# Optimization experiments

Hardware: AMD Instinct MI355X
Metric: run time of the kernel (lower is better)

## Reference

```python
import jax, jax.numpy as jnp
import numpy as np

B, N, D, H = 16, 512, 256, 8
E_PER = 16384  # edges per graph (avg degree 32)
BN_EPS = 1e-5


def _bn(x, g, b, m, v):
    # BatchNorm1d in eval mode: normalize with running stats
    return (x - m) * (g * jax.lax.rsqrt(v + BN_EPS)) + b


def setup_inputs() -> dict:
    key = jax.random.key(0)
    ks = jax.random.split(key, 32)
    E = B * E_PER
    w = lambda k, s: (jax.random.normal(k, s, jnp.float32) * 0.02)
    # block-diagonal edge list: indices within each graph + graph offset
    src = jax.random.randint(ks[1], (B, E_PER), 0, N)
    dst = jax.random.randint(ks[2], (B, E_PER), 0, N)
    off = (jnp.arange(B) * N)[:, None]
    inp = {
        "x": jax.random.normal(ks[0], (B * N, D), jnp.float32),
        "edge_rows": (src + off).reshape(-1).astype(jnp.int32),
        "edge_cols": (dst + off).reshape(-1).astype(jnp.int32),
        "edge_vals": jax.random.uniform(ks[3], (E,), jnp.float32) * 0.1,
        "w_gcn": w(ks[4], (D, D)),
        "in_proj_w": w(ks[5], (3 * D, D)),
        "in_proj_b": w(ks[6], (3 * D,)),
        "out_proj_w": w(ks[7], (D, D)),
        "out_proj_b": w(ks[8], (D,)),
        "w1": w(ks[9], (4 * D, D)),
        "b1": w(ks[10], (4 * D,)),
        "w2": w(ks[11], (D, 4 * D)),
        "b2": w(ks[12], (D,)),
        "batch_size": B,
        "num_nodes": N,
    }
    for i, name in enumerate(["bn1", "bn2", "bn3"]):
        k4 = jax.random.split(ks[13 + i], 4)
        inp[name + "_g"] = 1.0 + jax.random.uniform(k4[0], (D,), jnp.float32) * 0.1
        inp[name + "_b"] = w(k4[1], (D,))
        inp[name + "_m"] = w(k4[2], (D,))
        inp[name + "_v"] = 1.0 + jax.random.uniform(k4[3], (D,), jnp.float32) * 0.1
    return inp


def reference(x, edge_rows, edge_cols, edge_vals, w_gcn,
              in_proj_w, in_proj_b, out_proj_w, out_proj_b,
              bn1_g, bn1_b, bn1_m, bn1_v,
              bn2_g, bn2_b, bn2_m, bn2_v,
              bn3_g, bn3_b, bn3_m, bn3_v,
              w1, b1, w2, b2, batch_size, num_nodes):
    n_total = x.shape[0]
    dh = D // H
    # --- local GCN: linear -> sparse SpMM (gather/scatter) -> exact GELU ---
    hl = x @ w_gcn.T                                            # (BN, D)
    agg = jax.ops.segment_sum(edge_vals[:, None] * hl[edge_cols],
                              edge_rows, num_segments=n_total)   # (BN, D)
    h_local = jax.nn.gelu(agg, approximate=False)
    x = x + h_local
    x = _bn(x, bn1_g, bn1_b, bn1_m, bn1_v)
    # --- global multi-head self-attention per graph ---
    h = x.reshape(batch_size, num_nodes, D)
    qkv = jnp.einsum('bnd,ed->bne', h, in_proj_w) + in_proj_b    # (B, N, 3D)
    q, k, v = jnp.split(qkv, 3, axis=-1)
    q = q.reshape(batch_size, num_nodes, H, dh)
    k = k.reshape(batch_size, num_nodes, H, dh)
    v = v.reshape(batch_size, num_nodes, H, dh)
    scores = jnp.einsum('bqhd,bkhd->bhqk', q, k) / jnp.sqrt(jnp.float32(dh))
    attn = jax.nn.softmax(scores, axis=-1)
    ctx = jnp.einsum('bhqk,bkhd->bqhd', attn, v).reshape(batch_size, num_nodes, D)
    h_attn = (ctx @ out_proj_w.T + out_proj_b).reshape(n_total, D)
    x = x + h_attn
    x = _bn(x, bn2_g, bn2_b, bn2_m, bn2_v)
    # --- FFN ---
    h_ffn = jax.nn.gelu(x @ w1.T + b1, approximate=False) @ w2.T + b2
    x = x + h_ffn
    x = _bn(x, bn3_g, bn3_b, bn3_m, bn3_v)
    return x
```

## Files before the change

### kernel.cpp

```cpp
#include <hip/hip_runtime.h>
#include <hip/hip_bf16.h>
#include <math.h>

#define D_    256
#define NT_   8192
#define NN_   512
#define B_    16
#define H_    8
#define EPG_  16384
#define BN_EPS 1e-5f

typedef __attribute__((ext_vector_type(8))) short bx8;
typedef __attribute__((ext_vector_type(4))) float fx4;

__device__ __forceinline__ float gelu_exact(float x) {
    return 0.5f * x * (1.0f + erff(x * 0.70710678118654752f));
}

typedef __attribute__((address_space(1))) const unsigned int GU;
typedef __attribute__((address_space(3))) unsigned int LU;
__device__ __forceinline__ void gl_lds16(const void* g, void* l) {
    __builtin_amdgcn_global_load_lds((GU*)g, (LU*)l, 16, 0, 0);
}

template<int TM, int TN, int EPI, int OBF, int RBF>
__global__ __launch_bounds__(256)
void mgemm(const short* __restrict__ A, const short* __restrict__ Bw,
           const float* __restrict__ bias, void* __restrict__ Cout,
           int M, int N, int K,
           long sA, long sB, long sC, long sR,
           const void* __restrict__ resid,
           const float* __restrict__ bng, const float* __restrict__ bnb,
           const float* __restrict__ bnm, const float* __restrict__ bnv)
{
    constexpr int MR = TM / 32, NR = TN / 32;
    constexpr int IA = TM / 16, IB = TN / 16;
    __shared__ short As[TM][32];
    __shared__ short Bs[TN][32];
    const int bz = blockIdx.z;
    A  += (size_t)bz * sA;
    Bw += (size_t)bz * sB;
    const int bm = blockIdx.y * TM, bn = blockIdx.x * TN;
    const int tid = threadIdx.x;
    const int w = tid >> 6, lane = tid & 63;
    const int wm = w >> 1, wn = w & 1;
    const int fr = lane & 15, fk = (lane >> 4) << 3;
    const int srow = lane >> 2, scol = (lane & 3) << 3;
    fx4 acc[MR][NR] = {};

    for (int k0 = 0; k0 < K; k0 += 32) {
        __syncthreads();
        #pragma unroll
        for (int i = w; i < IA + IB; i += 4) {
            if (i < IA)
                gl_lds16(A + (size_t)(bm + i * 16 + srow) * K + k0 + scol,
                         (char*)As + i * 1024);
            else
                gl_lds16(Bw + (size_t)(bn + (i - IA) * 16 + srow) * K + k0 + scol,
                         (char*)Bs + (i - IA) * 1024);
        }
        __syncthreads();
        bx8 af[MR], bf[NR];
        #pragma unroll
        for (int m = 0; m < MR; ++m) af[m] = *(const bx8*)&As[wm * (TM / 2) + m * 16 + fr][fk];
        #pragma unroll
        for (int n = 0; n < NR; ++n) bf[n] = *(const bx8*)&Bs[wn * (TN / 2) + n * 16 + fr][fk];
        #pragma unroll
        for (int m = 0; m < MR; ++m)
            #pragma unroll
            for (int n = 0; n < NR; ++n)
                acc[m][n] = __builtin_amdgcn_mfma_f32_16x16x32_bf16(af[m], bf[n], acc[m][n], 0, 0, 0);
    }

    float* Cf = (float*)Cout + (size_t)bz * sC;
    __hip_bfloat16* Cb = (__hip_bfloat16*)Cout + (size_t)bz * sC;
    const float* Rf = (const float*)resid + (EPI >= 2 ? (size_t)bz * sR : 0);
    const __hip_bfloat16* Rb = (const __hip_bfloat16*)resid + (EPI >= 2 ? (size_t)bz * sR : 0);
    #pragma unroll
    for (int m = 0; m < MR; ++m) {
        #pragma unroll
        for (int n = 0; n < NR; ++n) {
            #pragma unroll
            for (int r = 0; r < 4; ++r) {
                const int gm = bm + wm * (TM / 2) + m * 16 + (lane >> 4) * 4 + r;
                const int gn = bn + wn * (TN / 2) + n * 16 + fr;
                float v = acc[m][n][r];
                if (bias) v += bias[gn];
                if (EPI == 1) v = gelu_exact(v);
                if (EPI == 2 || EPI == 3) {
                    const float rv = RBF ? __bfloat162float(Rb[(size_t)gm * N + gn])
                                         : Rf[(size_t)gm * N + gn];
                    if (EPI == 2) v += rv;
                    else          v = rv + gelu_exact(v);
                    v = (v - bnm[gn]) * (bng[gn] * rsqrtf(bnv[gn] + BN_EPS)) + bnb[gn];
                }
                if (OBF) Cb[(size_t)gm * N + gn] = __float2bfloat16(v);
                else     Cf[(size_t)gm * N + gn] = v;
            }
        }
    }
}

__device__ __forceinline__ void cv4(const float4 v, __hip_bfloat16* d) {
    __hip_bfloat162* dp = (__hip_bfloat162*)d;
    dp[0] = __hip_bfloat162(__float2bfloat16(v.x), __float2bfloat16(v.y));
    dp[1] = __hip_bfloat162(__float2bfloat16(v.z), __float2bfloat16(v.w));
}

__global__ __launch_bounds__(256)
void conv6(const float* __restrict__ x,  const float* __restrict__ wg,
           const float* __restrict__ iw, const float* __restrict__ ow,
           const float* __restrict__ w1, const float* __restrict__ w2,
           __hip_bfloat16* xb, __hip_bfloat16* wgb, __hip_bfloat16* iwb,
           __hip_bfloat16* owb, __hip_bfloat16* w1b, __hip_bfloat16* w2b)
{
    int i = blockIdx.x * 256 + threadIdx.x;
    const float* s; __hip_bfloat16* d; int o;
    if      (i < 524288) { s = x;  d = xb;  o = i; }
    else if (i < 540672) { s = wg; d = wgb; o = i - 524288; }
    else if (i < 589824) { s = iw; d = iwb; o = i - 540672; }
    else if (i < 606208) { s = ow; d = owb; o = i - 589824; }
    else if (i < 671744) { s = w1; d = w1b; o = i - 606208; }
    else                 { s = w2; d = w2b; o = i - 671744; }
    cv4(((const float4*)s)[o], d + (size_t)o * 4);
}

__global__ __launch_bounds__(256)
void convA(const float* __restrict__ s, __hip_bfloat16* __restrict__ d, int n4)
{
    int i = blockIdx.x * 256 + threadIdx.x;
    if (i >= n4) return;
    cv4(((const float4*)s)[i], d + (size_t)i * 4);
}

__global__ __launch_bounds__(256)
void build_S(const int* __restrict__ rows, const int* __restrict__ cols,
             const float* __restrict__ vals, float* __restrict__ SA)
{
    const int e = blockIdx.x * 256 + threadIdx.x;
    const int r = rows[e], c = cols[e];
    const int g = r >> 9;
    atomicAdd(&SA[((size_t)g << 18) + (size_t)(r & 511) * 512 + (c - (g << 9))], vals[e]);
}

__global__ __launch_bounds__(256)
void transp(const __hip_bfloat16* __restrict__ hl, __hip_bfloat16* __restrict__ hlB)
{
    __shared__ short T[64][72];
    const int nt = blockIdx.x, it = blockIdx.y, g = blockIdx.z;
    const int r0 = threadIdx.x >> 3, c8 = (threadIdx.x & 7) << 3;
    #pragma unroll
    for (int u = 0; u < 2; ++u) {
        const int r = r0 + u * 32;
        *(bx8*)&T[r][c8] = *(const bx8*)&hl[(size_t)(g * 512 + it * 64 + r) * 256 + nt * 64 + c8];
    }
    __syncthreads();
    #pragma unroll
    for (int u = 0; u < 2; ++u) {
        const int r = r0 + u * 32;
        bx8 o;
        #pragma unroll
        for (int j = 0; j < 8; ++j) o[j] = T[c8 + j][r];
        *(bx8*)&hlB[((size_t)(g * 256 + nt * 64 + r)) * 512 + it * 64 + c8] = o;
    }
}

__global__ __launch_bounds__(256, 1)
void attn_mfma(const short* __restrict__ qkv, __hip_bfloat16* __restrict__ ctx)
{
    const int qt = blockIdx.x & 7;
    const int h  = (blockIdx.x >> 3) & 7;
    const int b  = blockIdx.x >> 6;
    __shared__ short Ks[512][40];
    __shared__ short Vt[32][520];
    __shared__ short Ps[64][520];
    const int tid = threadIdx.x;
    const int lane = tid & 63, wq = tid >> 6;
    const short* base = qkv + (size_t)b * NN_ * 768;

    {
        const int d0 = (tid & 3) << 3;
        const int k0 = tid >> 2;
        #pragma unroll
        for (int rep = 0; rep < 8; ++rep) {
            const int key = k0 + rep * 64;
            *(bx8*)&Ks[key][d0] =
                *(const bx8*)(base + (size_t)key * 768 + 256 + h * 32 + d0);
        }
    }
    {
        const int d0 = (tid >> 6) << 3;
        const int k0 = tid & 63;
        #pragma unroll
        for (int rep = 0; rep < 8; ++rep) {
            const int key = k0 + rep * 64;
            bx8 vv = *(const bx8*)(base + (size_t)key * 768 + 512 + h * 32 + d0);
            #pragma unroll
            for (int j = 0; j < 8; ++j) Vt[d0 + j][key] = vv[j];
        }
    }
    const int fr = lane & 15, fk = (lane >> 4) << 3;
    const int qrow = qt * 64 + wq * 16 + fr;
    bx8 qf = *(const bx8*)(base + (size_t)qrow * 768 + h * 32 + fk);
    __syncthreads();

    fx4 sc[32];
    #pragma unroll
    for (int nt = 0; nt < 32; ++nt) {
        bx8 kf = *(const bx8*)&Ks[nt * 16 + fr][fk];
        fx4 z = {0.f, 0.f, 0.f, 0.f};
        sc[nt] = __builtin_amdgcn_mfma_f32_16x16x32_bf16(qf, kf, z, 0, 0, 0);
    }

    const float scale = 0.17677669529663687f;
    #pragma unroll
    for (int r = 0; r < 4; ++r) {
        float m = -1e30f;
        #pragma unroll
        for (int nt = 0; nt < 32; ++nt) m = fmaxf(m, sc[nt][r]);
        #pragma unroll
        for (int off = 1; off < 16; off <<= 1)
            m = fmaxf(m, __shfl_xor(m, off, 64));
        const float M = m * scale;
        float s = 0.f;
        #pragma unroll
        for (int nt = 0; nt < 32; ++nt) {
            const float p = __expf(sc[nt][r] * scale - M);
            sc[nt][r] = p;
            s += p;
        }
        #pragma unroll
        for (int off = 1; off < 16; off <<= 1) s += __shfl_xor(s, off, 64);
        const float inv = 1.0f / s;
        const int q = wq * 16 + (lane >> 4) * 4 + r;
        #pragma unroll
        for (int nt = 0; nt < 32; ++nt)
            *(__hip_bfloat16*)&Ps[q][nt * 16 + fr] = __float2bfloat16(sc[nt][r] * inv);
    }

    fx4 oacc[2] = {};
    #pragma unroll
    for (int step = 0; step < 16; ++step) {
        bx8 pf = *(const bx8*)&Ps[wq * 16 + fr][step * 32 + fk];
        #pragma unroll
        for (int nt = 0; nt < 2; ++nt) {
            bx8 vf = *(const bx8*)&Vt[nt * 16 + fr][step * 32 + fk];
            oacc[nt] = __builtin_amdgcn_mfma_f32_16x16x32_bf16(pf, vf, oacc[nt], 0, 0, 0);
        }
    }
    #pragma unroll
    for (int nt = 0; nt < 2; ++nt) {
        #pragma unroll
        for (int r = 0; r < 4; ++r) {
            const int q = qt * 64 + wq * 16 + (lane >> 4) * 4 + r;
            const int d = nt * 16 + fr;
            ctx[(size_t)(b * NN_ + q) * D_ + h * 32 + d] = __float2bfloat16(oacc[nt][r]);
        }
    }
}

extern "C" void kernel_launch(void* const* d_in, const int* in_sizes, int n_in,
                              void* d_out, int out_size, void* d_ws, size_t ws_size,
                              hipStream_t stream) {
    const float* x      = (const float*)d_in[0];
    const int*   erows  = (const int*)d_in[1];
    const int*   ecols  = (const int*)d_in[2];
    const float* evals  = (const float*)d_in[3];
    const float* w_gcn  = (const float*)d_in[4];
    const float* in_w   = (const float*)d_in[5];
    const float* in_b   = (const float*)d_in[6];
    const float* outw   = (const float*)d_in[7];
    const float* outb   = (const float*)d_in[8];
    const float* w1     = (const float*)d_in[9];
    const float* b1     = (const float*)d_in[10];
    const float* w2     = (const float*)d_in[11];
    const float* b2     = (const float*)d_in[12];
    const float* bn1g = (const float*)d_in[15], *bn1b = (const float*)d_in[16];
    const float* bn1m = (const float*)d_in[17], *bn1v = (const float*)d_in[18];
    const float* bn2g = (const float*)d_in[19], *bn2b = (const float*)d_in[20];
    const float* bn2m = (const float*)d_in[21], *bn2v = (const float*)d_in[22];
    const float* bn3g = (const float*)d_in[23], *bn3b = (const float*)d_in[24];
    const float* bn3m = (const float*)d_in[25], *bn3v = (const float*)d_in[26];

    short* wsS = (short*)d_ws;
    __hip_bfloat16* xb    = (__hip_bfloat16*)(wsS + 0);
    __hip_bfloat16* wgcnb = (__hip_bfloat16*)(wsS + 2097152);
    __hip_bfloat16* iwb   = (__hip_bfloat16*)(wsS + 2162688);
    __hip_bfloat16* owb   = (__hip_bfloat16*)(wsS + 2359296);
    __hip_bfloat16* w1b   = (__hip_bfloat16*)(wsS + 2424832);
    __hip_bfloat16* w2b   = (__hip_bfloat16*)(wsS + 2686976);
    short* hl   = wsS + 2949120;
    short* hlB  = wsS + 5046272;
    short* x1b  = wsS + 7143424;
    short* ctxb = wsS + 9240576;
    short* x2b  = wsS + 11337728;
    short* h1b  = wsS + 13434880;
    short* SAb  = wsS + 21823488;
    float* SA   = (float*)(wsS + 26017792);
    short* qkvb = wsS + 26017792;
    float* out  = (float*)d_out;

    dim3 blk(256);
    conv6<<<dim3(2880), blk, 0, stream>>>(x, w_gcn, in_w, outw, w1, w2,
                                          xb, wgcnb, iwb, owb, w1b, w2b);
    hipMemsetAsync(SA, 0, (size_t)16 * 512 * 512 * 4, stream);
    build_S<<<dim3(1024), blk, 0, stream>>>(erows, ecols, evals, SA);
    convA<<<dim3(4096), blk, 0, stream>>>(SA, (__hip_bfloat16*)SAb, 1048576);
    mgemm<64,64,0,1,0><<<dim3(4, 128), blk, 0, stream>>>((const short*)xb, (const short*)wgcnb,
        nullptr, hl, NT_, D_, D_, 0,0,0,0, nullptr, nullptr, nullptr, nullptr, nullptr);
    transp<<<dim3(4, 8, 16), blk, 0, stream>>>((const __hip_bfloat16*)hl, (__hip_bfloat16*)hlB);
    mgemm<64,64,3,1,0><<<dim3(4, 8, 16), blk, 0, stream>>>(SAb, hlB, nullptr, x1b,
        512, D_, 512, 262144, 131072, 131072, 131072,
        x, bn1g, bn1b, bn1m, bn1v);
    mgemm<128,64,0,1,0><<<dim3(12, 64), blk, 0, stream>>>(x1b, (const short*)iwb, in_b, qkvb,
        NT_, 3 * D_, D_, 0,0,0,0, nullptr, nullptr, nullptr, nullptr, nullptr);
    attn_mfma<<<dim3(1024), blk, 0, stream>>>(qkvb, (__hip_bfloat16*)ctxb);
    mgemm<64,64,2,1,1><<<dim3(4, 128), blk, 0, stream>>>(ctxb, (const short*)owb, outb, x2b,
        NT_, D_, D_, 0,0,0,0, x1b, bn2g, bn2b, bn2m, bn2v);
    mgemm<128,64,1,1,0><<<dim3(16, 64), blk, 0, stream>>>(x2b, (const short*)w1b, b1, h1b,
        NT_, 4 * D_, D_, 0,0,0,0, nullptr, nullptr, nullptr, nullptr, nullptr);
    mgemm<64,64,2,0,1><<<dim3(4, 128), blk, 0, stream>>>(h1b, (const short*)w2b, b2, out,
        NT_, D_, 4 * D_, 0,0,0,0, x2b, bn3g, bn3b, bn3m, bn3v);
}
```

Before: 258.0 us.

## Deepen GEMM K-step to 64 with XOR-swizzled LDS, enlarge tiles, swizzle attention blocks

The GEMM kernel now stages 64-wide K slices per iteration into LDS, using an XOR swizzle on 16-byte chunks to avoid bank conflicts, and issues two MFMA sub-steps per barrier pair. This halves the number of synchronisation rounds and should reduce LDS conflicts. The QKV and FFN-up GEMMs switch to 128x128 tiles for more register reuse, at the cost of fewer blocks. The attention kernel remaps block indices so that consecutively launched blocks spread across different graphs and heads.

```diff
diff --git a/kernel.cpp b/kernel.cpp
--- a/kernel.cpp
+++ b/kernel.cpp
@@ -34,9 +34,9 @@
            const float* __restrict__ bnm, const float* __restrict__ bnv)
 {
     constexpr int MR = TM / 32, NR = TN / 32;
-    constexpr int IA = TM / 16, IB = TN / 16;
-    __shared__ short As[TM][32];
-    __shared__ short Bs[TN][32];
+    constexpr int NIA = TM / 8, NIB = TN / 8;
+    __shared__ short As[TM][64];
+    __shared__ short Bs[TN][64];
     const int bz = blockIdx.z;
     A  += (size_t)bz * sA;
     Bw += (size_t)bz * sB;
@@ -44,32 +44,43 @@
     const int tid = threadIdx.x;
     const int w = tid >> 6, lane = tid & 63;
     const int wm = w >> 1, wn = w & 1;
-    const int fr = lane & 15, fk = (lane >> 4) << 3;
-    const int srow = lane >> 2, scol = (lane & 3) << 3;
+    const int fr = lane & 15;
+    const int srow = lane >> 3;
+    const int scol = (((lane & 7) ^ (srow & 7)) << 3);
     fx4 acc[MR][NR] = {};
 
-    for (int k0 = 0; k0 < K; k0 += 32) {
+    for (int k0 = 0; k0 < K; k0 += 64) {
         __syncthreads();
         #pragma unroll
-        for (int i = w; i < IA + IB; i += 4) {
-            if (i < IA)
-                gl_lds16(A + (size_t)(bm + i * 16 + srow) * K + k0 + scol,
+        for (int i = w; i < NIA + NIB; i += 4) {
+            if (i < NIA)
+                gl_lds16(A + (size_t)(bm + i * 8 + srow) * K + k0 + scol,
                          (char*)As + i * 1024);
             else
-                gl_lds16(Bw + (size_t)(bn + (i - IA) * 16 + srow) * K + k0 + scol,
-                         (char*)Bs + (i - IA) * 1024);
+                gl_lds16(Bw + (size_t)(bn + (i - NIA) * 8 + srow) * K + k0 + scol,
+                         (char*)Bs + (i - NIA) * 1024);
         }
         __syncthreads();
-        bx8 af[MR], bf[NR];
-        #pragma unroll
-        for (int m = 0; m < MR; ++m) af[m] = *(const bx8*)&As[wm * (TM / 2) + m * 16 + fr][fk];
-        #pragma unroll
-        for (int n = 0; n < NR; ++n) bf[n] = *(const bx8*)&Bs[wn * (TN / 2) + n * 16 + fr][fk];
-        #pragma unroll
-        for (int m = 0; m < MR; ++m)
-            #pragma unroll
-            for (int n = 0; n < NR; ++n)
-                acc[m][n] = __builtin_amdgcn_mfma_f32_16x16x32_bf16(af[m], bf[n], acc[m][n], 0, 0, 0);
+        #pragma unroll
+        for (int ks = 0; ks < 2; ++ks) {
+            const int sl = (ks << 2) | (lane >> 4);
+            bx8 af[MR], bf[NR];
+            #pragma unroll
+            for (int m = 0; m < MR; ++m) {
+                const int row = wm * (TM / 2) + m * 16 + fr;
+                af[m] = *(const bx8*)&As[row][(sl ^ (row & 7)) << 3];
+            }
+            #pragma unroll
+            for (int n = 0; n < NR; ++n) {
+                const int row = wn * (TN / 2) + n * 16 + fr;
+                bf[n] = *(const bx8*)&Bs[row][(sl ^ (row & 7)) << 3];
+            }
+            #pragma unroll
+            for (int m = 0; m < MR; ++m)
+                #pragma unroll
+                for (int n = 0; n < NR; ++n)
+                    acc[m][n] = __builtin_amdgcn_mfma_f32_16x16x32_bf16(af[m], bf[n], acc[m][n], 0, 0, 0);
+        }
     }
 
     float* Cf = (float*)Cout + (size_t)bz * sC;
@@ -168,9 +179,10 @@
 __global__ __launch_bounds__(256, 1)
 void attn_mfma(const short* __restrict__ qkv, __hip_bfloat16* __restrict__ ctx)
 {
-    const int qt = blockIdx.x & 7;
-    const int h  = (blockIdx.x >> 3) & 7;
-    const int b  = blockIdx.x >> 6;
+    const int swz = (blockIdx.x & 7) * 128 + (blockIdx.x >> 3);
+    const int qt = swz & 7;
+    const int h  = (swz >> 3) & 7;
+    const int b  = swz >> 6;
     __shared__ short Ks[512][40];
     __shared__ short Vt[32][520];
     __shared__ short Ps[64][520];
@@ -312,12 +324,12 @@
     mgemm<64,64,3,1,0><<<dim3(4, 8, 16), blk, 0, stream>>>(SAb, hlB, nullptr, x1b,
         512, D_, 512, 262144, 131072, 131072, 131072,
         x, bn1g, bn1b, bn1m, bn1v);
-    mgemm<128,64,0,1,0><<<dim3(12, 64), blk, 0, stream>>>(x1b, (const short*)iwb, in_b, qkvb,
+    mgemm<128,128,0,1,0><<<dim3(6, 64), blk, 0, stream>>>(x1b, (const short*)iwb, in_b, qkvb,
         NT_, 3 * D_, D_, 0,0,0,0, nullptr, nullptr, nullptr, nullptr, nullptr);
     attn_mfma<<<dim3(1024), blk, 0, stream>>>(qkvb, (__hip_bfloat16*)ctxb);
     mgemm<64,64,2,1,1><<<dim3(4, 128), blk, 0, stream>>>(ctxb, (const short*)owb, outb, x2b,
         NT_, D_, D_, 0,0,0,0, x1b, bn2g, bn2b, bn2m, bn2v);
-    mgemm<128,64,1,1,0><<<dim3(16, 64), blk, 0, stream>>>(x2b, (const short*)w1b, b1, h1b,
+    mgemm<128,128,1,1,0><<<dim3(8, 64), blk, 0, stream>>>(x2b, (const short*)w1b, b1, h1b,
         NT_, 4 * D_, D_, 0,0,0,0, nullptr, nullptr, nullptr, nullptr, nullptr);
     mgemm<64,64,2,0,1><<<dim3(4, 128), blk, 0, stream>>>(h1b, (const short*)w2b, b2, out,
         NT_, D_, 4 * D_, 0,0,0,0, x2b, bn3g, bn3b, bn3m, bn3v);
```

New measurement: 278.3 us. +7.9%, slower.
